# Optimization experiments

Hardware: AMD Instinct MI355X
Metric: run time of the kernel (lower is better)

Reference implementation:

```python
import jax, jax.numpy as jnp
import numpy as np

INPUT_SIZE, HIDDEN, OUTPUT = 6, 64, 3
B, T = 4096, 512


def setup_inputs() -> dict:
    key = jax.random.key(0)
    ks = jax.random.split(key, 12)
    s = 1.0 / np.sqrt(HIDDEN)  # torch LSTM/Linear default init scale
    u = lambda k, shape: jax.random.uniform(k, shape, jnp.float32, -s, s)
    return {
        "x": jax.random.normal(ks[0], (B, T, INPUT_SIZE), jnp.float32),
        "Wih0": u(ks[1], (4 * HIDDEN, INPUT_SIZE)),
        "Whh0": u(ks[2], (4 * HIDDEN, HIDDEN)),
        "bih0": u(ks[3], (4 * HIDDEN,)),
        "bhh0": u(ks[4], (4 * HIDDEN,)),
        "Wih1": u(ks[5], (4 * HIDDEN, HIDDEN)),
        "Whh1": u(ks[6], (4 * HIDDEN, HIDDEN)),
        "bih1": u(ks[7], (4 * HIDDEN,)),
        "bhh1": u(ks[8], (4 * HIDDEN,)),
        "Wfc": u(ks[9], (OUTPUT, HIDDEN)),
        "bfc": u(ks[10], (OUTPUT,)),
    }


def _lstm_layer(x, Wih, Whh, bih, bhh):
    # x: [B, T, F] -> hidden sequence [B, T, H]; torch gate order i,f,g,o
    Bn = x.shape[0]
    H = Whh.shape[1]
    b = bih + bhh
    # precompute input projections for all steps: [T, B, 4H]
    gx = jnp.einsum('btf,gf->tbg', x, Wih) + b

    def step(carry, gxt):
        h, c = carry
        gates = gxt + h @ Whh.T
        i, f, g, o = jnp.split(gates, 4, axis=-1)
        i, f, o = jax.nn.sigmoid(i), jax.nn.sigmoid(f), jax.nn.sigmoid(o)
        g = jnp.tanh(g)
        c = f * c + i * g
        h = o * jnp.tanh(c)
        return (h, c), h

    h0 = jnp.zeros((Bn, H), x.dtype)
    c0 = jnp.zeros((Bn, H), x.dtype)
    (_, _), hs = jax.lax.scan(step, (h0, c0), gx)  # hs: [T, B, H]
    return hs.transpose(1, 0, 2)


def reference(x, Wih0, Whh0, bih0, bhh0, Wih1, Whh1, bih1, bhh1, Wfc, bfc):
    h1 = _lstm_layer(x, Wih0, Whh0, bih0, bhh0)
    h2 = _lstm_layer(h1, Wih1, Whh1, bih1, bhh1)
    last = h2[:, -1, :]              # [B, H]
    return last @ Wfc.T + bfc        # [B, OUTPUT]
```

## Files before the change

### kernel.cpp

```cpp
#include <hip/hip_runtime.h>

#define H    64
#define TT   512
#define NB   16
#define OUTD 3
#define BTOT 4096
#define INF  6

typedef _Float16 f16;
typedef _Float16 f16x8 __attribute__((ext_vector_type(8)));
typedef float    f32x4 __attribute__((ext_vector_type(4)));
typedef float    f32x2 __attribute__((ext_vector_type(2)));

#define AS 168

#define LOG2E 1.44269504088896340736f
#define KSC   (2.0f * LOG2E)

static __device__ __forceinline__ f32x2 pk_fma(f32x2 a, f32x2 b, f32x2 c) {
#if __has_builtin(__builtin_elementwise_fma)
    return __builtin_elementwise_fma(a, b, c);
#else
    f32x2 r; r.x = __builtin_fmaf(a.x, b.x, c.x); r.y = __builtin_fmaf(a.y, b.y, c.y);
    return r;
#endif
}

static __device__ __forceinline__ f32x2 pk_min(f32x2 a, f32x2 b) {
#if __has_builtin(__builtin_elementwise_min)
    return __builtin_elementwise_min(a, b);
#else
    f32x2 r; r.x = fminf(a.x, b.x); r.y = fminf(a.y, b.y);
    return r;
#endif
}

__device__ __forceinline__ f32x2 lstm_cell2(f32x2 ai, f32x2 af, f32x2 ag, f32x2 ao,
                                            f32x2& C) {
    f32x2 ei, ef, eg, eo;
    ei.x = __builtin_amdgcn_exp2f(ai.x); ei.y = __builtin_amdgcn_exp2f(ai.y);
    ef.x = __builtin_amdgcn_exp2f(af.x); ef.y = __builtin_amdgcn_exp2f(af.y);
    eg.x = __builtin_amdgcn_exp2f(ag.x); eg.y = __builtin_amdgcn_exp2f(ag.y);
    eo.x = __builtin_amdgcn_exp2f(ao.x); eo.y = __builtin_amdgcn_exp2f(ao.y);
    f32x2 A  = ei + 1.0f;
    f32x2 F  = ef + 1.0f;
    f32x2 Bp = eg + 1.0f;
    f32x2 G  = eg - 1.0f;
    f32x2 P  = A * Bp;
    f32x2 PF = P * F;
    f32x2 r1; r1.x = __builtin_amdgcn_rcpf(PF.x); r1.y = __builtin_amdgcn_rcpf(PF.y);
    f32x2 n1 = ef * C * P;
    f32x2 t2 = ei * G * F;
    f32x2 k2 = {KSC, KSC};
    C = pk_fma(k2, t2, n1) * r1;
    f32x2 clim = {126.0f, 126.0f};
    f32x2 Cc = pk_min(C, clim);
    f32x2 ec; ec.x = __builtin_amdgcn_exp2f(Cc.x); ec.y = __builtin_amdgcn_exp2f(Cc.y);
    f32x2 D2 = (eo + 1.0f) * (ec + 1.0f);
    f32x2 r2; r2.x = __builtin_amdgcn_rcpf(D2.x); r2.y = __builtin_amdgcn_rcpf(D2.y);
    return eo * (ec - 1.0f) * r2;
}

__launch_bounds__(512, 2)
__global__ void lstm_ws(const float* __restrict__ x,
                        const float* __restrict__ Wih0, const float* __restrict__ Whh0,
                        const float* __restrict__ bih0, const float* __restrict__ bhh0,
                        const float* __restrict__ Wih1, const float* __restrict__ Whh1,
                        const float* __restrict__ bih1, const float* __restrict__ bhh1,
                        const float* __restrict__ Wfc,  const float* __restrict__ bfc,
                        float* __restrict__ out)
{
    __shared__ __align__(16) f16 Phi[2][NB * AS];
    __shared__ float hfin[NB][H + 1];

    const int t    = threadIdx.x;
    const int u    = t & 255;
    const int role = t >> 8;
    const int wv   = u >> 6;
    const int l15  = u & 15;
    const int q    = (u >> 4) & 3;
    const int jj   = 16 * wv + l15;
    const int b0   = blockIdx.x * NB;
    const int ar   = l15 * AS;
    const int ko   = q * 8;

    {
        f16* ph = &Phi[0][0];
        for (int idx = t; idx < 2 * NB * AS; idx += 512) ph[idx] = (f16)0.0f;
    }
    __syncthreads();

    const bool loader = (role == 0) && (u < NB * INF);
    const int  xb = u / INF;
    const int  xf = u - xb * INF;
    if (loader)
        Phi[0][xb * AS + 128 + xf] = (f16)x[((size_t)(b0 + xb) * TT) * INF + xf];
    __syncthreads();

    if (role == 0) {
        f16x8 wh0[2][4];
        f16x8 wx0[4];
        f32x4 bC0[4];
        #pragma unroll
        for (int g = 0; g < 4; ++g) {
            const float sc = (g == 2) ? (2.0f * LOG2E) : LOG2E;
            const int n = 64 * g + jj;
            #pragma unroll
            for (int kt = 0; kt < 2; ++kt) {
                f16x8 v;
                #pragma unroll
                for (int j = 0; j < 8; ++j)
                    v[j] = (f16)(Whh0[n * H + kt * 32 + q * 8 + j] * sc);
                wh0[kt][g] = v;
            }
            f16x8 vx;
            #pragma unroll
            for (int j = 0; j < 8; ++j)
                vx[j] = (q == 0 && j < INF) ? (f16)(Wih0[n * INF + j] * sc) : (f16)0.0f;
            wx0[g] = vx;
            const float bu = (bih0[64 * g + jj] + bhh0[64 * g + jj]) * sc;
            bC0[g] = (f32x4){bu, bu, bu, bu};
        }
        f32x2 c01 = {0.f, 0.f}, c23 = {0.f, 0.f};
        float xpre = 0.0f;

        auto stepL0 = [&](f16* __restrict__ AH, f16* __restrict__ BH, int s) {
            if (loader) {
                const int tn = (s + 1 < TT) ? (s + 1) : (TT - 1);
                xpre = x[((size_t)(b0 + xb) * TT + tn) * INF + xf];
            }
            f16x8 a0 = *(const f16x8*)&AH[ar + 0   + ko];
            f16x8 a1 = *(const f16x8*)&AH[ar + 32  + ko];
            f16x8 ax = *(const f16x8*)&BH[ar + 128 + ko];
            __builtin_amdgcn_s_setprio(1);
            f32x4 accA[4];
            #pragma unroll
            for (int g = 0; g < 4; ++g) {
                f32x4 acc;
                acc = __builtin_amdgcn_mfma_f32_16x16x32_f16(a0, wh0[0][g], bC0[g], 0, 0, 0);
                acc = __builtin_amdgcn_mfma_f32_16x16x32_f16(a1, wh0[1][g], acc, 0, 0, 0);
                acc = __builtin_amdgcn_mfma_f32_16x16x32_f16(ax, wx0[g],    acc, 0, 0, 0);
                accA[g] = acc;
            }
            __builtin_amdgcn_s_setprio(0);
            f32x2 h01 = lstm_cell2((f32x2){accA[0][0], accA[0][1]},
                                   (f32x2){accA[1][0], accA[1][1]},
                                   (f32x2){accA[2][0], accA[2][1]},
                                   (f32x2){accA[3][0], accA[3][1]}, c01);
            f32x2 h23 = lstm_cell2((f32x2){accA[0][2], accA[0][3]},
                                   (f32x2){accA[1][2], accA[1][3]},
                                   (f32x2){accA[2][2], accA[2][3]},
                                   (f32x2){accA[3][2], accA[3][3]}, c23);
            BH[(q * 4 + 0) * AS + jj] = (f16)h01.x;
            BH[(q * 4 + 1) * AS + jj] = (f16)h01.y;
            BH[(q * 4 + 2) * AS + jj] = (f16)h23.x;
            BH[(q * 4 + 3) * AS + jj] = (f16)h23.y;
            if (loader) AH[xb * AS + 128 + xf] = (f16)xpre;
            __syncthreads();
        };

        for (int s = 0; s < TT; s += 2) {
            stepL0(Phi[1], Phi[0], s);
            stepL0(Phi[0], Phi[1], s + 1);
        }
        __syncthreads();
    } else {
        f16x8 wi1[2][4];
        f16x8 wh1[2][4];
        f32x4 bC1[4];
        #pragma unroll
        for (int g = 0; g < 4; ++g) {
            const float sc = (g == 2) ? (2.0f * LOG2E) : LOG2E;
            const int n = 64 * g + jj;
            #pragma unroll
            for (int kt = 0; kt < 2; ++kt) {
                f16x8 v1, v2;
                #pragma unroll
                for (int j = 0; j < 8; ++j) {
                    const int k = kt * 32 + q * 8 + j;
                    v1[j] = (f16)(Wih1[n * H + k] * sc);
                    v2[j] = (f16)(Whh1[n * H + k] * sc);
                }
                wi1[kt][g] = v1; wh1[kt][g] = v2;
            }
            const float bu = (bih1[64 * g + jj] + bhh1[64 * g + jj]) * sc;
            bC1[g] = (f32x4){bu, bu, bu, bu};
        }
        f32x2 c01 = {0.f, 0.f}, c23 = {0.f, 0.f};

        __syncthreads();

        auto stepL1 = [&](f16* __restrict__ AH, f16* __restrict__ BH, int s) {
            f16x8 n0 = *(const f16x8*)&AH[ar + 0  + ko];
            f16x8 n1 = *(const f16x8*)&AH[ar + 32 + ko];
            f16x8 r0 = *(const f16x8*)&BH[ar + 64 + ko];
            f16x8 r1 = *(const f16x8*)&BH[ar + 96 + ko];
            f32x4 accB[4];
            #pragma unroll
            for (int g = 0; g < 4; ++g) {
                f32x4 acc;
                acc = __builtin_amdgcn_mfma_f32_16x16x32_f16(n0, wi1[0][g], bC1[g], 0, 0, 0);
                acc = __builtin_amdgcn_mfma_f32_16x16x32_f16(n1, wi1[1][g], acc, 0, 0, 0);
                acc = __builtin_amdgcn_mfma_f32_16x16x32_f16(r0, wh1[0][g], acc, 0, 0, 0);
                acc = __builtin_amdgcn_mfma_f32_16x16x32_f16(r1, wh1[1][g], acc, 0, 0, 0);
                accB[g] = acc;
            }
            f32x2 h01 = lstm_cell2((f32x2){accB[0][0], accB[0][1]},
                                   (f32x2){accB[1][0], accB[1][1]},
                                   (f32x2){accB[2][0], accB[2][1]},
                                   (f32x2){accB[3][0], accB[3][1]}, c01);
            f32x2 h23 = lstm_cell2((f32x2){accB[0][2], accB[0][3]},
                                   (f32x2){accB[1][2], accB[1][3]},
                                   (f32x2){accB[2][2], accB[2][3]},
                                   (f32x2){accB[3][2], accB[3][3]}, c23);
            AH[(q * 4 + 0) * AS + 64 + jj] = (f16)h01.x;
            AH[(q * 4 + 1) * AS + 64 + jj] = (f16)h01.y;
            AH[(q * 4 + 2) * AS + 64 + jj] = (f16)h23.x;
            AH[(q * 4 + 3) * AS + 64 + jj] = (f16)h23.y;
            if (s == TT) {
                hfin[q * 4 + 0][jj] = h01.x;
                hfin[q * 4 + 1][jj] = h01.y;
                hfin[q * 4 + 2][jj] = h23.x;
                hfin[q * 4 + 3][jj] = h23.y;
            }
            __syncthreads();
        };

        for (int s = 1; s <= TT; s += 2) {
            stepL1(Phi[0], Phi[1], s);
            stepL1(Phi[1], Phi[0], s + 1);
        }
    }

    if (t < NB * OUTD) {
        const int b = t / OUTD;
        const int o = t - b * OUTD;
        float a = bfc[o];
        #pragma unroll
        for (int j = 0; j < H; ++j)
            a += Wfc[o * H + j] * hfin[b][j];
        out[(size_t)(b0 + b) * OUTD + o] = a;
    }
}

extern "C" void kernel_launch(void* const* d_in, const int* in_sizes, int n_in,
                              void* d_out, int out_size, void* d_ws, size_t ws_size,
                              hipStream_t stream) {
    const float* x    = (const float*)d_in[0];
    const float* Wih0 = (const float*)d_in[1];
    const float* Whh0 = (const float*)d_in[2];
    const float* bih0 = (const float*)d_in[3];
    const float* bhh0 = (const float*)d_in[4];
    const float* Wih1 = (const float*)d_in[5];
    const float* Whh1 = (const float*)d_in[6];
    const float* bih1 = (const float*)d_in[7];
    const float* bhh1 = (const float*)d_in[8];
    const float* Wfc  = (const float*)d_in[9];
    const float* bfc  = (const float*)d_in[10];

    dim3 grid(BTOT / NB);
    dim3 block(512);
    lstm_ws<<<grid, block, 0, stream>>>(x, Wih0, Whh0, bih0, bhh0,
                                        Wih1, Whh1, bih1, bhh1,
                                        Wfc, bfc, (float*)d_out);
}
```

Baseline: 416.2 us.

## Load x directly into registers and split layer-1 MFMA chains for ILP

```diff
diff --git a/kernel.cpp b/kernel.cpp
--- a/kernel.cpp
+++ b/kernel.cpp
@@ -90,13 +90,6 @@
     }
     __syncthreads();
 
-    const bool loader = (role == 0) && (u < NB * INF);
-    const int  xb = u / INF;
-    const int  xf = u - xb * INF;
-    if (loader)
-        Phi[0][xb * AS + 128 + xf] = (f16)x[((size_t)(b0 + xb) * TT) * INF + xf];
-    __syncthreads();
-
     if (role == 0) {
         f16x8 wh0[2][4];
         f16x8 wx0[4];
@@ -122,27 +115,36 @@
             bC0[g] = (f32x4){bu, bu, bu, bu};
         }
         f32x2 c01 = {0.f, 0.f}, c23 = {0.f, 0.f};
-        float xpre = 0.0f;
+
+        const float* xrow = &x[(size_t)(b0 + l15) * TT * INF];
+        f32x2 xc0, xc1, xc2;
+        xc0 = *(const f32x2*)&xrow[0];
+        xc1 = *(const f32x2*)&xrow[2];
+        xc2 = *(const f32x2*)&xrow[4];
+        __syncthreads();
 
         auto stepL0 = [&](f16* __restrict__ AH, f16* __restrict__ BH, int s) {
-            if (loader) {
-                const int tn = (s + 1 < TT) ? (s + 1) : (TT - 1);
-                xpre = x[((size_t)(b0 + xb) * TT + tn) * INF + xf];
-            }
-            f16x8 a0 = *(const f16x8*)&AH[ar + 0   + ko];
-            f16x8 a1 = *(const f16x8*)&AH[ar + 32  + ko];
-            f16x8 ax = *(const f16x8*)&BH[ar + 128 + ko];
-            __builtin_amdgcn_s_setprio(1);
+            f16x8 ax;
+            ax[0] = (f16)xc0.x; ax[1] = (f16)xc0.y;
+            ax[2] = (f16)xc1.x; ax[3] = (f16)xc1.y;
+            ax[4] = (f16)xc2.x; ax[5] = (f16)xc2.y;
+            ax[6] = (f16)0.0f;  ax[7] = (f16)0.0f;
+            const int tn = (s + 1 < TT) ? (s + 1) : (TT - 1);
+            const float* xp = &xrow[(size_t)tn * INF];
+            f32x2 xn0 = *(const f32x2*)&xp[0];
+            f32x2 xn1 = *(const f32x2*)&xp[2];
+            f32x2 xn2 = *(const f32x2*)&xp[4];
+            f16x8 a0 = *(const f16x8*)&AH[ar + 0  + ko];
+            f16x8 a1 = *(const f16x8*)&AH[ar + 32 + ko];
             f32x4 accA[4];
             #pragma unroll
             for (int g = 0; g < 4; ++g) {
                 f32x4 acc;
-                acc = __builtin_amdgcn_mfma_f32_16x16x32_f16(a0, wh0[0][g], bC0[g], 0, 0, 0);
+                acc = __builtin_amdgcn_mfma_f32_16x16x32_f16(ax, wx0[g],    bC0[g], 0, 0, 0);
+                acc = __builtin_amdgcn_mfma_f32_16x16x32_f16(a0, wh0[0][g], acc, 0, 0, 0);
                 acc = __builtin_amdgcn_mfma_f32_16x16x32_f16(a1, wh0[1][g], acc, 0, 0, 0);
-                acc = __builtin_amdgcn_mfma_f32_16x16x32_f16(ax, wx0[g],    acc, 0, 0, 0);
                 accA[g] = acc;
             }
-            __builtin_amdgcn_s_setprio(0);
             f32x2 h01 = lstm_cell2((f32x2){accA[0][0], accA[0][1]},
                                    (f32x2){accA[1][0], accA[1][1]},
                                    (f32x2){accA[2][0], accA[2][1]},
@@ -155,7 +157,7 @@
             BH[(q * 4 + 1) * AS + jj] = (f16)h01.y;
             BH[(q * 4 + 2) * AS + jj] = (f16)h23.x;
             BH[(q * 4 + 3) * AS + jj] = (f16)h23.y;
-            if (loader) AH[xb * AS + 128 + xf] = (f16)xpre;
+            xc0 = xn0; xc1 = xn1; xc2 = xn2;
             __syncthreads();
         };
 
@@ -186,8 +188,10 @@
             const float bu = (bih1[64 * g + jj] + bhh1[64 * g + jj]) * sc;
             bC1[g] = (f32x4){bu, bu, bu, bu};
         }
+        const f32x4 z4 = {0.f, 0.f, 0.f, 0.f};
         f32x2 c01 = {0.f, 0.f}, c23 = {0.f, 0.f};
 
+        __syncthreads();
         __syncthreads();
 
         auto stepL1 = [&](f16* __restrict__ AH, f16* __restrict__ BH, int s) {
@@ -198,12 +202,12 @@
             f32x4 accB[4];
             #pragma unroll
             for (int g = 0; g < 4; ++g) {
-                f32x4 acc;
-                acc = __builtin_amdgcn_mfma_f32_16x16x32_f16(n0, wi1[0][g], bC1[g], 0, 0, 0);
-                acc = __builtin_amdgcn_mfma_f32_16x16x32_f16(n1, wi1[1][g], acc, 0, 0, 0);
-                acc = __builtin_amdgcn_mfma_f32_16x16x32_f16(r0, wh1[0][g], acc, 0, 0, 0);
-                acc = __builtin_amdgcn_mfma_f32_16x16x32_f16(r1, wh1[1][g], acc, 0, 0, 0);
-                accB[g] = acc;
+                f32x4 cN, cR;
+                cN = __builtin_amdgcn_mfma_f32_16x16x32_f16(n0, wi1[0][g], bC1[g], 0, 0, 0);
+                cR = __builtin_amdgcn_mfma_f32_16x16x32_f16(r0, wh1[0][g], z4, 0, 0, 0);
+                cN = __builtin_amdgcn_mfma_f32_16x16x32_f16(n1, wi1[1][g], cN, 0, 0, 0);
+                cR = __builtin_amdgcn_mfma_f32_16x16x32_f16(r1, wh1[1][g], cR, 0, 0, 0);
+                accB[g] = cN + cR;
             }
             f32x2 h01 = lstm_cell2((f32x2){accB[0][0], accB[0][1]},
                                    (f32x2){accB[1][0], accB[1][1]},
```

New measurement: 439.3 us. 5.6% more time.
